# Optimization experiments

Hardware: AMD Instinct MI355X
Metric: run time of the kernel (lower is better)

Reference implementation:

```python
import jax, jax.numpy as jnp
import numpy as np

B, H, W, C = 4, 64, 64, 512
LN_EPS = 1e-3  # keras LayerNormalization default epsilon


def setup_inputs() -> dict:
    key = jax.random.key(0)
    ks = jax.random.split(key, 10)
    s = 1.0 / np.sqrt(C)
    return {
        "x": jax.random.normal(ks[0], (B, H, W, C), dtype=jnp.float32),
        "ln_g": jnp.ones((C,), jnp.float32),
        "ln_b": jnp.zeros((C,), jnp.float32),
        "Wq": jax.random.normal(ks[1], (C, C), jnp.float32) * s,
        "bq": jnp.zeros((C,), jnp.float32),
        "Wk": jax.random.normal(ks[2], (C, C), jnp.float32) * s,
        "bk": jnp.zeros((C,), jnp.float32),
        "Wv": jax.random.normal(ks[3], (C, C), jnp.float32) * s,
        "bv": jnp.zeros((C,), jnp.float32),
        "Wp": jax.random.normal(ks[4], (C, C), jnp.float32) * s,
        "bp": jnp.zeros((C,), jnp.float32),
    }


def reference(x, ln_g, ln_b, Wq, bq, Wk, bk, Wv, bv, Wp, bp):
    b, h_, w_, c = x.shape
    n = h_ * w_
    # LayerNorm over channel axis (keras default axis=-1, eps=1e-3)
    mu = jnp.mean(x, axis=-1, keepdims=True)
    var = jnp.var(x, axis=-1, keepdims=True)
    hn = (x - mu) * jax.lax.rsqrt(var + LN_EPS) * ln_g + ln_b
    hf = hn.reshape(b, n, c)
    q = hf @ Wq + bq  # [b, n, c]
    k = hf @ Wk + bk
    v = hf @ Wv + bv
    scale = 1.0 / jnp.sqrt(jnp.asarray(c, x.dtype))
    scores = jnp.einsum("bqc,bkc->bqk", q, k) * scale  # [b, n, n]
    attn = jax.nn.softmax(scores, axis=-1)
    o = jnp.einsum("bqk,bkc->bqc", attn, v)  # [b, n, c]
    o = o @ Wp + bp
    return x + o.reshape(b, h_, w_, c)
```

## Files before the change

### kernel.cpp

```cpp
#include <hip/hip_runtime.h>
#include <cstdint>
#include <cmath>

typedef unsigned short u16;
typedef __attribute__((ext_vector_type(8))) short short8;
typedef __attribute__((ext_vector_type(4))) float f32x4;

#define BB 4
#define NTOK 4096
#define CDIM 512
#define NROWS (BB * NTOK)
#define QSCALE 0.0441941738241592f

__device__ __forceinline__ u16 f2bf(float f) {
  union { float f; uint32_t u; } v; v.f = f;
  return (u16)((v.u + 0x7fffu + ((v.u >> 16) & 1u)) >> 16);
}

__device__ __forceinline__ float bf2f(u16 u) {
  union { uint32_t u; float f; } v; v.u = (uint32_t)u << 16;
  return v.f;
}

__device__ __forceinline__ f32x4 mfma16(short8 a, short8 b, f32x4 c) {
  return __builtin_amdgcn_mfma_f32_16x16x32_bf16(a, b, c, 0, 0, 0);
}

__device__ __forceinline__ void gload16(const u16* g, u16* l) {
  __builtin_amdgcn_global_load_lds(
      (const __attribute__((address_space(1))) void*)g,
      (__attribute__((address_space(3))) void*)l, 16, 0, 0);
}

__global__ __launch_bounds__(256) void ln_kernel(const float* __restrict__ x,
                                                 const float* __restrict__ gam,
                                                 const float* __restrict__ bet,
                                                 u16* __restrict__ hn) {
  int row = blockIdx.x * 4 + (threadIdx.x >> 6);
  int lane = threadIdx.x & 63;
  const float4* xr = (const float4*)(x + (size_t)row * CDIM);
  float4 a0 = xr[lane];
  float4 a1 = xr[lane + 64];
  float s = a0.x + a0.y + a0.z + a0.w + a1.x + a1.y + a1.z + a1.w;
  float ss = a0.x * a0.x + a0.y * a0.y + a0.z * a0.z + a0.w * a0.w +
             a1.x * a1.x + a1.y * a1.y + a1.z * a1.z + a1.w * a1.w;
#pragma unroll
  for (int j = 0; j < 6; ++j) {
    s += __shfl_xor(s, 1 << j);
    ss += __shfl_xor(ss, 1 << j);
  }
  float mu = s * (1.0f / CDIM);
  float var = ss * (1.0f / CDIM) - mu * mu;
  float rs = rsqrtf(var + 1e-3f);
  const float4* g4 = (const float4*)gam;
  const float4* b4 = (const float4*)bet;
  float4 g0 = g4[lane], g1 = g4[lane + 64];
  float4 c0 = b4[lane], c1 = b4[lane + 64];
  u16* out = hn + (size_t)row * CDIM;
  ushort4 o0, o1;
  o0.x = f2bf((a0.x - mu) * rs * g0.x + c0.x);
  o0.y = f2bf((a0.y - mu) * rs * g0.y + c0.y);
  o0.z = f2bf((a0.z - mu) * rs * g0.z + c0.z);
  o0.w = f2bf((a0.w - mu) * rs * g0.w + c0.w);
  o1.x = f2bf((a1.x - mu) * rs * g1.x + c1.x);
  o1.y = f2bf((a1.y - mu) * rs * g1.y + c1.y);
  o1.z = f2bf((a1.z - mu) * rs * g1.z + c1.z);
  o1.w = f2bf((a1.w - mu) * rs * g1.w + c1.w);
  *(ushort4*)(out + lane * 4) = o0;
  *(ushort4*)(out + 256 + lane * 4) = o1;
}

__global__ __launch_bounds__(256) void wconv_kernel(
    const float* __restrict__ w0, const float* __restrict__ w1,
    const float* __restrict__ w2, const float* __restrict__ w3,
    const float* __restrict__ bq, const float* __restrict__ bk,
    const float* __restrict__ bv,
    u16* __restrict__ wt, float* __restrict__ bqkv) {
  __shared__ __align__(16) u16 tile[64][65];
  int which = blockIdx.z;
  const float* W = (which == 0) ? w0 : (which == 1) ? w1 : (which == 2) ? w2 : w3;
  float wscale = (which == 0) ? QSCALE : 1.0f;
  u16* WT = wt + (size_t)which * CDIM * CDIM;
  int kb = blockIdx.x * 64, nb = blockIdx.y * 64;
  int t = threadIdx.x;
  if (kb == 0 && which < 3 && t < 64) {
    const float* bs = (which == 0) ? bq : (which == 1) ? bk : bv;
    bqkv[which * CDIM + nb + t] = bs[nb + t] * wscale;
  }
#pragma unroll
  for (int i = 0; i < 16; ++i) {
    int idx = t + i * 256;
    int r = idx >> 6, c = idx & 63;
    tile[r][c] = f2bf(W[(size_t)(kb + r) * CDIM + nb + c] * wscale);
  }
  __syncthreads();
#pragma unroll
  for (int i = 0; i < 16; ++i) {
    int idx = t + i * 256;
    int r = idx >> 6, c = idx & 63;
    WT[(size_t)(nb + r) * CDIM + kb + c] = tile[c][r];
  }
}

__global__ __launch_bounds__(256) void vtrans_kernel(const u16* __restrict__ v,
                                                     int ld,
                                                     u16* __restrict__ vt) {
  __shared__ __align__(16) u16 tile[64][65];
  int nb = blockIdx.x * 64;
  int cb = blockIdx.y * 64;
  int b = blockIdx.z;
  int t = threadIdx.x;
  const u16* src = v + ((size_t)b * NTOK + nb) * ld + cb;
#pragma unroll
  for (int i = 0; i < 16; ++i) {
    int idx = t + i * 256;
    int r = idx >> 6, c = idx & 63;
    tile[r][c] = src[(size_t)r * ld + c];
  }
  __syncthreads();
  u16* dst = vt + ((size_t)b * CDIM + cb) * NTOK + nb;
#pragma unroll
  for (int i = 0; i < 16; ++i) {
    int idx = t + i * 256;
    int r = idx >> 6, c = idx & 63;
    dst[(size_t)r * NTOK + c] = tile[c][r];
  }
}

template <int MODE, int LOGSPLIT>
__global__ __launch_bounds__(512) void gemm256_kernel(
    const u16* __restrict__ A, int lda, size_t az,
    const u16* __restrict__ Bt, int ldb, size_t bz,
    const float* __restrict__ bias,
    const float* __restrict__ lsum, int lz,
    u16* __restrict__ outp, int ldo, size_t oz, size_t koz,
    int K) {
  __shared__ __align__(16) u16 lds[8][8192];
  int t = threadIdx.x;
  int w = t >> 6, lane = t & 63;
  int lr = lane & 15, lg = lane >> 4;
  int wr = w >> 2, wc = w & 3;
  int gx = gridDim.x, gy = gridDim.y;
  int nwg = gx * gy * (int)gridDim.z;
  int nlin = blockIdx.x + gx * (blockIdx.y + gy * blockIdx.z);
  int cpx = nwg >> 3;
  int swz = (nlin & 7) * cpx + (nlin >> 3);
  int bx = swz % gx;
  int rem = swz / gx;
  int by = rem % gy;
  int bz2 = rem / gy;
  int batch = bz2 >> LOGSPLIT;
  int kq = bz2 & ((1 << LOGSPLIT) - 1);
  size_t aoff = az * (size_t)batch + (size_t)kq * K;
  size_t boff = bz * (size_t)batch + (size_t)kq * K;
  size_t ooff = oz * (size_t)batch + koz * (size_t)kq;
  int lsrow0 = lz * batch;
  int mbase = by * 256, nbase = bx * 256;
  const f32x4 fz = {0.f, 0.f, 0.f, 0.f};
  f32x4 acc[8][4];
#pragma unroll
  for (int m = 0; m < 8; ++m)
#pragma unroll
    for (int n2 = 0; n2 < 4; ++n2) acc[m][n2] = fz;

  int srow = t >> 3;
  int scol = ((t & 7) ^ (srow & 7)) * 8;
  const u16* ga = A + aoff + (size_t)(mbase + srow) * lda + scol;
  const u16* gb = Bt + boff + (size_t)(nbase + srow) * ldb + scol;
  int pse0 = (lg ^ (lr & 7)) * 8;
  int pse1 = pse0 ^ 32;

#define STG_A(h, tile, d)                                              \
  {                                                                    \
    const u16* s_ = ga + (size_t)((h)*128) * lda + (tile)*64;          \
    u16* d_ = &lds[(d)*4 + (h)][0] + w * 512;                          \
    gload16(s_, d_);                                                   \
    gload16(s_ + (size_t)64 * lda, d_ + 4096);                        \
  }
#define STG_B(h, tile, d)                                              \
  {                                                                    \
    const u16* s_ = gb + (size_t)((h)*128) * ldb + (tile)*64;          \
    u16* d_ = &lds[(d)*4 + 2 + (h)][0] + w * 512;                      \
    gload16(s_, d_);                                                   \
    gload16(s_ + (size_t)64 * ldb, d_ + 4096);                        \
  }

#define RD_A(dst, d, mh)                                               \
  {                                                                    \
    const u16* p_ = &lds[(d)*4 + wr][0] + (((mh)*64 + lr) << 6);       \
    _Pragma("unroll") for (int m = 0; m < 4; ++m) {                    \
      dst[m * 2 + 0] = *(const short8*)(p_ + (m << 10) + pse0);        \
      dst[m * 2 + 1] = *(const short8*)(p_ + (m << 10) + pse1);        \
    }                                                                  \
  }
#define RD_B(dst, d, nh)                                               \
  {                                                                    \
    const u16* p_ = &lds[(d)*4 + 2 + (wc >> 1)][0] +                   \
                    (((wc & 1) * 64 + (nh)*32 + lr) << 6);             \
    _Pragma("unroll") for (int n2 = 0; n2 < 2; ++n2) {                 \
      dst[n2 * 2 + 0] = *(const short8*)(p_ + (n2 << 10) + pse0);      \
      dst[n2 * 2 + 1] = *(const short8*)(p_ + (n2 << 10) + pse1);      \
    }                                                                  \
  }

#define PHEND                                                          \
  asm volatile("" ::: "memory");                                       \
  __builtin_amdgcn_sched_barrier(0);                                   \
  __builtin_amdgcn_s_barrier();                                        \
  asm volatile("s_waitcnt lgkmcnt(0)" ::: "memory");                   \
  __builtin_amdgcn_sched_barrier(0);

#define VM2 asm volatile("s_waitcnt vmcnt(2)" ::: "memory");
#define VM0 asm volatile("s_waitcnt vmcnt(0)" ::: "memory");

#define MM(X, Y, mq, nq)                                               \
  __builtin_amdgcn_s_setprio(1);                                       \
  _Pragma("unroll") for (int m = 0; m < 4; ++m)                        \
      _Pragma("unroll") for (int n2 = 0; n2 < 2; ++n2)                 \
          _Pragma("unroll") for (int ks = 0; ks < 2; ++ks)             \
              acc[(mq)*4 + m][(nq)*2 + n2] =                           \
                  mfma16(X[m * 2 + ks], Y[n2 * 2 + ks],                \
                         acc[(mq)*4 + m][(nq)*2 + n2]);                \
  __builtin_amdgcn_s_setprio(0);

  short8 Af[8], Ag[8], Bf[4], Bg[4];
  int niter = K >> 7;

  STG_A(0, 0, 0); STG_A(1, 0, 0); STG_B(0, 0, 0); STG_B(1, 0, 0);
  STG_B(0, 1, 1);
  VM2;
  __builtin_amdgcn_s_barrier();
  asm volatile("" ::: "memory");
  __builtin_amdgcn_sched_barrier(0);

  for (int j = 0; j < niter; ++j) {
    int T1i = 2 * j + 1, T2i = 2 * j + 2, T3i = 2 * j + 3;
    bool more = (j + 1 < niter);
    RD_A(Af, 0, 0); RD_B(Bf, 0, 0);
    STG_B(1, T1i, 1);
    PHEND; MM(Af, Bf, 0, 0);
    RD_B(Bg, 0, 1);
    STG_A(0, T1i, 1);
    PHEND; MM(Af, Bg, 0, 1);
    RD_A(Ag, 0, 1);
    STG_A(1, T1i, 1);
    PHEND; MM(Ag, Bg, 1, 1);
    if (more) { STG_B(0, T2i, 0); VM2; } else { VM0; }
    PHEND; MM(Ag, Bf, 1, 0);
    RD_A(Af, 1, 0); RD_B(Bf, 1, 0);
    if (more) STG_B(1, T2i, 0);
    PHEND; MM(Af, Bf, 0, 0);
    RD_B(Bg, 1, 1);
    if (more) STG_A(0, T2i, 0);
    PHEND; MM(Af, Bg, 0, 1);
    RD_A(Ag, 1, 1);
    if (more) STG_A(1, T2i, 0);
    PHEND; MM(Ag, Bg, 1, 1);
    if (more) { STG_B(0, T3i, 1); VM2; } else { VM0; }
    PHEND; MM(Ag, Bf, 1, 0);
  }
#undef MM
#undef VM2
#undef VM0
#undef PHEND
#undef RD_A
#undef RD_B
#undef STG_A
#undef STG_B

  u16* op = outp + ooff;
#pragma unroll
  for (int m = 0; m < 8; ++m) {
    int grow = mbase + wr * 128 + m * 16 + lg * 4;
    float rl[4];
    if (MODE == 3) {
#pragma unroll
      for (int r = 0; r < 4; ++r)
        rl[r] = 1.0f / lsum[lsrow0 + grow + r];
    }
#pragma unroll
    for (int n2 = 0; n2 < 4; ++n2) {
      int gcol = nbase + wc * 64 + n2 * 16 + lr;
      float bnc = (MODE == 0) ? bias[gcol] : 0.f;
#pragma unroll
      for (int r = 0; r < 4; ++r) {
        size_t idx = (size_t)(grow + r) * ldo + gcol;
        float val = acc[m][n2][r];
        if (MODE == 0) {
          op[idx] = f2bf(val + bnc);
        } else if (MODE == 2) {
          op[idx] = f2bf(val);
        } else {
          op[idx] = f2bf(val * rl[r]);
        }
      }
    }
  }
}

__global__ __launch_bounds__(256) void gemm_fin_kernel(
    const u16* __restrict__ A, int lda,
    const u16* __restrict__ Bt, int ldb,
    const float* __restrict__ bias, const float* __restrict__ res,
    float* __restrict__ outp, int ldo, int K) {
  __shared__ __align__(16) u16 Als[2][128 * 32];
  __shared__ __align__(16) u16 Bls[2][128 * 32];
  int t = threadIdx.x;
  int w = t >> 6, lane = t & 63;
  int lr = lane & 15, lg = lane >> 4;
  int wr = w >> 1, wc = w & 1;
  int mbase = blockIdx.y * 128, nbase = blockIdx.x * 128;
  const f32x4 fz = {0.f, 0.f, 0.f, 0.f};
  f32x4 acc[4][4];
#pragma unroll
  for (int m = 0; m < 4; ++m)
#pragma unroll
    for (int n = 0; n < 4; ++n) acc[m][n] = fz;

  int scol = (((t & 3) ^ ((t >> 2) & 3) ^ ((t >> 4) & 1)) * 8);
  const u16* ga0 = A + (size_t)(mbase + (t >> 2)) * lda + scol;
  const u16* gb0 = Bt + (size_t)(nbase + (t >> 2)) * ldb + scol;
  int rsA = (lg ^ (lr & 3) ^ ((lr >> 2) & 1)) * 8;

#define STAGE(buf, ko)                                                 \
  {                                                                    \
    gload16(ga0 + (ko), &Als[buf][w * 512]);                           \
    gload16(ga0 + (size_t)64 * lda + (ko), &Als[buf][w * 512 + 2048]); \
    gload16(gb0 + (ko), &Bls[buf][w * 512]);                           \
    gload16(gb0 + (size_t)64 * ldb + (ko), &Bls[buf][w * 512 + 2048]); \
  }

  int nk = K >> 5;
  STAGE(0, 0);
  STAGE(1, 32);
  int cur = 0;
  for (int kt = 0; kt < nk; ++kt) {
    if (kt + 1 < nk) {
      asm volatile("s_waitcnt vmcnt(4)" ::: "memory");
    } else {
      asm volatile("s_waitcnt vmcnt(0)" ::: "memory");
    }
    __builtin_amdgcn_s_barrier();
    asm volatile("" ::: "memory");
    __builtin_amdgcn_sched_barrier(0);
    short8 af[4], bfr[4];
#pragma unroll
    for (int m = 0; m < 4; ++m)
      af[m] = *(const short8*)(&Als[cur][(wr * 64 + m * 16 + lr) * 32 + rsA]);
#pragma unroll
    for (int n = 0; n < 4; ++n)
      bfr[n] = *(const short8*)(&Bls[cur][(wc * 64 + n * 16 + lr) * 32 + rsA]);
#pragma unroll
    for (int m = 0; m < 4; ++m)
#pragma unroll
      for (int n = 0; n < 4; ++n)
        acc[m][n] = mfma16(af[m], bfr[n], acc[m][n]);
    asm volatile("s_waitcnt lgkmcnt(0)" ::: "memory");
    __builtin_amdgcn_s_barrier();
    asm volatile("" ::: "memory");
    if (kt + 2 < nk) STAGE(cur, (kt + 2) * 32);
    cur ^= 1;
  }
#undef STAGE

#pragma unroll
  for (int m = 0; m < 4; ++m) {
    int grow = mbase + wr * 64 + m * 16 + lg * 4;
#pragma unroll
    for (int n = 0; n < 4; ++n) {
      int gcol = nbase + wc * 64 + n * 16 + lr;
      float bnc = bias[gcol];
#pragma unroll
      for (int r = 0; r < 4; ++r) {
        size_t idx = (size_t)(grow + r) * ldo + gcol;
        outp[idx] = acc[m][n][r] + bnc + res[idx];
      }
    }
  }
}

__global__ __launch_bounds__(256) void softmax_kernel(u16* __restrict__ S,
                                                      float* __restrict__ lsum) {
  int row = blockIdx.x * 4 + (threadIdx.x >> 6);
  int lane = threadIdx.x & 63;
  u16* Sr = S + (size_t)row * NTOK;
  short8 d[8];
#pragma unroll
  for (int i = 0; i < 8; ++i)
    d[i] = *(const short8*)(Sr + i * 512 + lane * 8);
  float mx = -1e30f;
#pragma unroll
  for (int i = 0; i < 8; ++i)
#pragma unroll
    for (int j = 0; j < 8; ++j) mx = fmaxf(mx, bf2f((u16)d[i][j]));
#pragma unroll
  for (int j = 0; j < 6; ++j) mx = fmaxf(mx, __shfl_xor(mx, 1 << j));
  float sum = 0.f;
#pragma unroll
  for (int i = 0; i < 8; ++i) {
    short8 o;
#pragma unroll
    for (int j = 0; j < 8; ++j) {
      float p = __expf(bf2f((u16)d[i][j]) - mx);
      sum += p;
      o[j] = (short)f2bf(p);
    }
    *(short8*)(Sr + i * 512 + lane * 8) = o;
  }
#pragma unroll
  for (int j = 0; j < 6; ++j) sum += __shfl_xor(sum, 1 << j);
  if (lane == 0) lsum[row] = sum;
}

__global__ __launch_bounds__(256) void addp2_kernel(const u16* __restrict__ p,
                                                    size_t ss,
                                                    u16* __restrict__ ob) {
  size_t i = ((size_t)blockIdx.x * 256 + threadIdx.x) * 8;
  short8 a0 = *(const short8*)(p + i);
  short8 a1 = *(const short8*)(p + ss + i);
  short8 o;
#pragma unroll
  for (int j = 0; j < 8; ++j)
    o[j] = (short)f2bf(bf2f((u16)a0[j]) + bf2f((u16)a1[j]));
  *(short8*)(ob + i) = o;
}

extern "C" void kernel_launch(void* const* d_in, const int* in_sizes, int n_in,
                              void* d_out, int out_size, void* d_ws, size_t ws_size,
                              hipStream_t stream) {
  (void)in_sizes; (void)n_in; (void)out_size;
  const float* x    = (const float*)d_in[0];
  const float* ln_g = (const float*)d_in[1];
  const float* ln_b = (const float*)d_in[2];
  const float* Wq   = (const float*)d_in[3];
  const float* bq   = (const float*)d_in[4];
  const float* Wk   = (const float*)d_in[5];
  const float* bk   = (const float*)d_in[6];
  const float* Wv   = (const float*)d_in[7];
  const float* bv   = (const float*)d_in[8];
  const float* Wp   = (const float*)d_in[9];
  const float* bp   = (const float*)d_in[10];

  const size_t MB = 1024ull * 1024ull;
  const size_t KB = 1024ull;
  char* ws = (char*)d_ws;
  u16* wt     = (u16*)(ws);
  float* bqkv = (float*)(ws + 2 * MB);
  float* ls   = (float*)(ws + 2 * MB + 64 * KB);
  u16* hn     = (u16*)(ws + 4 * MB);
  u16* qkv    = (u16*)(ws + 20 * MB);
  u16* vt     = (u16*)(ws + 68 * MB);
  bool full = ws_size >= 212 * MB;
  u16* S    = (u16*)(ws + 84 * MB);
  u16* part = (u16*)(ws + 4 * MB);
  u16* ob   = full ? vt : (u16*)(ws + 116 * MB);

  const float* nullf = nullptr;

  hipLaunchKernelGGL(wconv_kernel, dim3(8, 8, 4), dim3(256), 0, stream,
                     Wq, Wk, Wv, Wp, bq, bk, bv, wt, bqkv);
  hipLaunchKernelGGL(ln_kernel, dim3(NROWS / 4), dim3(256), 0, stream,
                     x, ln_g, ln_b, hn);
  hipLaunchKernelGGL((gemm256_kernel<0, 0>), dim3(6, 64, 1), dim3(512), 0,
                     stream, hn, CDIM, (size_t)0, wt, CDIM, (size_t)0,
                     bqkv, nullf, 0, qkv, 3 * CDIM, (size_t)0, (size_t)0, CDIM);
  hipLaunchKernelGGL(vtrans_kernel, dim3(64, 8, 4), dim3(256), 0, stream,
                     qkv + 2 * CDIM, 3 * CDIM, vt);

  if (full) {
    hipLaunchKernelGGL((gemm256_kernel<2, 0>), dim3(16, 16, 4), dim3(512), 0,
                       stream, qkv, 3 * CDIM, (size_t)NTOK * 3 * CDIM,
                       qkv + CDIM, 3 * CDIM, (size_t)NTOK * 3 * CDIM,
                       nullf, nullf, 0,
                       S, NTOK, (size_t)NTOK * NTOK, (size_t)0, CDIM);
    hipLaunchKernelGGL(softmax_kernel, dim3(4 * NTOK / 4), dim3(256), 0, stream,
                       S, ls);
    hipLaunchKernelGGL((gemm256_kernel<3, 1>), dim3(2, 16, 8), dim3(512), 0,
                       stream, S, NTOK, (size_t)NTOK * NTOK,
                       vt, NTOK, (size_t)CDIM * NTOK,
                       nullf, ls, NTOK,
                       part, CDIM, (size_t)NTOK * CDIM,
                       (size_t)NROWS * CDIM, NTOK / 2);
    hipLaunchKernelGGL(addp2_kernel, dim3(NROWS * CDIM / 2048), dim3(256), 0,
                       stream, part, (size_t)NROWS * CDIM, ob);
  } else {
    for (int p = 0; p < 4; ++p) {
      const u16* qp  = qkv + (size_t)p * NTOK * 3 * CDIM;
      const u16* kp  = qp + CDIM;
      const u16* vtp = vt + (size_t)p * CDIM * NTOK;
      u16* obp = ob + (size_t)p * NTOK * CDIM;
      float* lp = ls + (size_t)p * NTOK;
      hipLaunchKernelGGL((gemm256_kernel<2, 0>), dim3(16, 16, 1), dim3(512), 0,
                         stream, qp, 3 * CDIM, (size_t)0, kp, 3 * CDIM,
                         (size_t)0, nullf, nullf, 0,
                         S, NTOK, (size_t)0, (size_t)0, CDIM);
      hipLaunchKernelGGL(softmax_kernel, dim3(NTOK / 4), dim3(256), 0, stream,
                         S, lp);
      hipLaunchKernelGGL((gemm256_kernel<3, 0>), dim3(2, 16, 1), dim3(512), 0,
                         stream, S, NTOK, (size_t)0, vtp, NTOK, (size_t)0,
                         nullf, lp, 0,
                         obp, CDIM, (size_t)0, (size_t)0, NTOK);
    }
  }
  hipLaunchKernelGGL(gemm_fin_kernel, dim3(4, 128), dim3(256), 0, stream,
                     ob, CDIM, wt + 3 * CDIM * CDIM, CDIM,
                     bp, x, (float*)d_out, CDIM, CDIM);
}
```

Before: 278.9 us.

## Fold output projection into V weights and fuse softmax exp into QK GEMM epilogue

Precomputes Wv·Wp in a small GEMM so the V projection produces already-projected values. This removes the final output-projection GEMM, and the split-K reduction kernel now also adds the bias and residual. The QK^T GEMM epilogue applies exp directly, with no max subtraction, and writes per-tile partial row sums. A small reduction kernel then combines those sums, which removes the separate softmax pass over the full score matrix. Skipping the max subtraction risks overflow when scores are large, and folding the weights changes the rounding order.

```diff
diff --git a/kernel.cpp b/kernel.cpp
--- a/kernel.cpp
+++ b/kernel.cpp
@@ -10,6 +10,7 @@
 #define NTOK 4096
 #define CDIM 512
 #define NROWS (BB * NTOK)
+#define SLOT ((size_t)CDIM * CDIM)
 #define QSCALE 0.0441941738241592f
 
 __device__ __forceinline__ u16 f2bf(float f) {
@@ -74,18 +75,28 @@
     const float* __restrict__ w0, const float* __restrict__ w1,
     const float* __restrict__ w2, const float* __restrict__ w3,
     const float* __restrict__ bq, const float* __restrict__ bk,
-    const float* __restrict__ bv,
     u16* __restrict__ wt, float* __restrict__ bqkv) {
   __shared__ __align__(16) u16 tile[64][65];
   int which = blockIdx.z;
   const float* W = (which == 0) ? w0 : (which == 1) ? w1 : (which == 2) ? w2 : w3;
   float wscale = (which == 0) ? QSCALE : 1.0f;
-  u16* WT = wt + (size_t)which * CDIM * CDIM;
+  const int slotmap[4] = {2, 3, 0, 1};
+  u16* WT = wt + (size_t)slotmap[which] * SLOT;
   int kb = blockIdx.x * 64, nb = blockIdx.y * 64;
   int t = threadIdx.x;
-  if (kb == 0 && which < 3 && t < 64) {
-    const float* bs = (which == 0) ? bq : (which == 1) ? bk : bv;
+  if (kb == 0 && which < 2 && t < 64) {
+    const float* bs = (which == 0) ? bq : bk;
     bqkv[which * CDIM + nb + t] = bs[nb + t] * wscale;
+  }
+  if (which == 2) {
+#pragma unroll
+    for (int i = 0; i < 16; ++i) {
+      int idx = t + i * 256;
+      int r = idx >> 6, c = idx & 63;
+      WT[(size_t)(kb + r) * CDIM + nb + c] =
+          f2bf(W[(size_t)(kb + r) * CDIM + nb + c]);
+    }
+    return;
   }
 #pragma unroll
   for (int i = 0; i < 16; ++i) {
@@ -100,6 +111,15 @@
     int r = idx >> 6, c = idx & 63;
     WT[(size_t)(nb + r) * CDIM + kb + c] = tile[c][r];
   }
+}
+
+__global__ __launch_bounds__(256) void bvp_kernel(const float* __restrict__ bv,
+                                                  const float* __restrict__ Wp,
+                                                  float* __restrict__ bqkv) {
+  int m = blockIdx.x * 256 + threadIdx.x;
+  float s = 0.f;
+  for (int k = 0; k < CDIM; ++k) s += bv[k] * Wp[(size_t)k * CDIM + m];
+  bqkv[2 * CDIM + m] = s;
 }
 
 __global__ __launch_bounds__(256) void vtrans_kernel(const u16* __restrict__ v,
@@ -132,7 +152,7 @@
     const u16* __restrict__ A, int lda, size_t az,
     const u16* __restrict__ Bt, int ldb, size_t bz,
     const float* __restrict__ bias,
-    const float* __restrict__ lsum, int lz,
+    float* __restrict__ lsum, int lz,
     u16* __restrict__ outp, int ldo, size_t oz, size_t koz,
     int K) {
   __shared__ __align__(16) u16 lds[8][8192];
@@ -269,6 +289,35 @@
 #undef STG_B
 
   u16* op = outp + ooff;
+  if (MODE == 2) {
+    __syncthreads();
+    float* redf = (float*)&lds[0][0];
+#pragma unroll
+    for (int m = 0; m < 8; ++m) {
+#pragma unroll
+      for (int r = 0; r < 4; ++r) {
+        int rowl = wr * 128 + m * 16 + lg * 4 + r;
+        float part = 0.f;
+#pragma unroll
+        for (int n2 = 0; n2 < 4; ++n2) {
+          int gcol = nbase + wc * 64 + n2 * 16 + lr;
+          float p = __expf(acc[m][n2][r]);
+          u16 pb = f2bf(p);
+          op[(size_t)(mbase + rowl) * ldo + gcol] = pb;
+          part += bf2f(pb);
+        }
+        redf[rowl * 65 + wc * 16 + lr] = part;
+      }
+    }
+    __syncthreads();
+    if (t < 256) {
+      float s = 0.f;
+#pragma unroll 8
+      for (int j2 = 0; j2 < 64; ++j2) s += redf[t * 65 + j2];
+      lsum[((size_t)bx * gridDim.z + batch) * (size_t)lz + mbase + t] = s;
+    }
+    return;
+  }
 #pragma unroll
   for (int m = 0; m < 8; ++m) {
     int grow = mbase + wr * 128 + m * 16 + lg * 4;
@@ -288,8 +337,6 @@
         float val = acc[m][n2][r];
         if (MODE == 0) {
           op[idx] = f2bf(val + bnc);
-        } else if (MODE == 2) {
-          op[idx] = f2bf(val);
         } else {
           op[idx] = f2bf(val * rl[r]);
         }
@@ -298,11 +345,9 @@
   }
 }
 
-__global__ __launch_bounds__(256) void gemm_fin_kernel(
-    const u16* __restrict__ A, int lda,
-    const u16* __restrict__ Bt, int ldb,
-    const float* __restrict__ bias, const float* __restrict__ res,
-    float* __restrict__ outp, int ldo, int K) {
+__global__ __launch_bounds__(256) void gemm_w_kernel(
+    const u16* __restrict__ A, const u16* __restrict__ Bt,
+    u16* __restrict__ outp) {
   __shared__ __align__(16) u16 Als[2][128 * 32];
   __shared__ __align__(16) u16 Bls[2][128 * 32];
   int t = threadIdx.x;
@@ -318,19 +363,19 @@
     for (int n = 0; n < 4; ++n) acc[m][n] = fz;
 
   int scol = (((t & 3) ^ ((t >> 2) & 3) ^ ((t >> 4) & 1)) * 8);
-  const u16* ga0 = A + (size_t)(mbase + (t >> 2)) * lda + scol;
-  const u16* gb0 = Bt + (size_t)(nbase + (t >> 2)) * ldb + scol;
+  const u16* ga0 = A + (size_t)(mbase + (t >> 2)) * CDIM + scol;
+  const u16* gb0 = Bt + (size_t)(nbase + (t >> 2)) * CDIM + scol;
   int rsA = (lg ^ (lr & 3) ^ ((lr >> 2) & 1)) * 8;
 
-#define STAGE(buf, ko)                                                 \
-  {                                                                    \
-    gload16(ga0 + (ko), &Als[buf][w * 512]);                           \
-    gload16(ga0 + (size_t)64 * lda + (ko), &Als[buf][w * 512 + 2048]); \
-    gload16(gb0 + (ko), &Bls[buf][w * 512]);                           \
-    gload16(gb0 + (size_t)64 * ldb + (ko), &Bls[buf][w * 512 + 2048]); \
-  }
-
-  int nk = K >> 5;
+#define STAGE(buf, ko)                                                  \
+  {                                                                     \
+    gload16(ga0 + (ko), &Als[buf][w * 512]);                            \
+    gload16(ga0 + (size_t)64 * CDIM + (ko), &Als[buf][w * 512 + 2048]); \
+    gload16(gb0 + (ko), &Bls[buf][w * 512]);                            \
+    gload16(gb0 + (size_t)64 * CDIM + (ko), &Bls[buf][w * 512 + 2048]); \
+  }
+
+  int nk = CDIM >> 5;
   STAGE(0, 0);
   STAGE(1, 32);
   int cur = 0;
@@ -369,60 +414,35 @@
 #pragma unroll
     for (int n = 0; n < 4; ++n) {
       int gcol = nbase + wc * 64 + n * 16 + lr;
-      float bnc = bias[gcol];
-#pragma unroll
-      for (int r = 0; r < 4; ++r) {
-        size_t idx = (size_t)(grow + r) * ldo + gcol;
-        outp[idx] = acc[m][n][r] + bnc + res[idx];
-      }
-    }
-  }
-}
-
-__global__ __launch_bounds__(256) void softmax_kernel(u16* __restrict__ S,
-                                                      float* __restrict__ lsum) {
-  int row = blockIdx.x * 4 + (threadIdx.x >> 6);
-  int lane = threadIdx.x & 63;
-  u16* Sr = S + (size_t)row * NTOK;
-  short8 d[8];
-#pragma unroll
-  for (int i = 0; i < 8; ++i)
-    d[i] = *(const short8*)(Sr + i * 512 + lane * 8);
-  float mx = -1e30f;
-#pragma unroll
-  for (int i = 0; i < 8; ++i)
-#pragma unroll
-    for (int j = 0; j < 8; ++j) mx = fmaxf(mx, bf2f((u16)d[i][j]));
-#pragma unroll
-  for (int j = 0; j < 6; ++j) mx = fmaxf(mx, __shfl_xor(mx, 1 << j));
-  float sum = 0.f;
-#pragma unroll
-  for (int i = 0; i < 8; ++i) {
-    short8 o;
-#pragma unroll
-    for (int j = 0; j < 8; ++j) {
-      float p = __expf(bf2f((u16)d[i][j]) - mx);
-      sum += p;
-      o[j] = (short)f2bf(p);
-    }
-    *(short8*)(Sr + i * 512 + lane * 8) = o;
-  }
-#pragma unroll
-  for (int j = 0; j < 6; ++j) sum += __shfl_xor(sum, 1 << j);
-  if (lane == 0) lsum[row] = sum;
-}
-
-__global__ __launch_bounds__(256) void addp2_kernel(const u16* __restrict__ p,
-                                                    size_t ss,
-                                                    u16* __restrict__ ob) {
+#pragma unroll
+      for (int r = 0; r < 4; ++r)
+        outp[(size_t)(grow + r) * CDIM + gcol] = f2bf(acc[m][n][r]);
+    }
+  }
+}
+
+__global__ __launch_bounds__(256) void lred_kernel(const float* __restrict__ lsp,
+                                                   float* __restrict__ ls,
+                                                   size_t stride) {
+  size_t r = (size_t)blockIdx.x * 256 + threadIdx.x;
+  float s = 0.f;
+#pragma unroll
+  for (int b = 0; b < 16; ++b) s += lsp[b * stride + r];
+  ls[r] = s;
+}
+
+__global__ __launch_bounds__(256) void addfin_kernel(const u16* __restrict__ p,
+                                                     size_t ss,
+                                                     const float* __restrict__ bp,
+                                                     const float* __restrict__ x,
+                                                     float* __restrict__ out) {
   size_t i = ((size_t)blockIdx.x * 256 + threadIdx.x) * 8;
   short8 a0 = *(const short8*)(p + i);
   short8 a1 = *(const short8*)(p + ss + i);
-  short8 o;
+  int col = (int)(i & (CDIM - 1));
 #pragma unroll
   for (int j = 0; j < 8; ++j)
-    o[j] = (short)f2bf(bf2f((u16)a0[j]) + bf2f((u16)a1[j]));
-  *(short8*)(ob + i) = o;
+    out[i + j] = bf2f((u16)a0[j]) + bf2f((u16)a1[j]) + bp[col + j] + x[i + j];
 }
 
 extern "C" void kernel_launch(void* const* d_in, const int* in_sizes, int n_in,
@@ -445,25 +465,30 @@
   const size_t KB = 1024ull;
   char* ws = (char*)d_ws;
   u16* wt     = (u16*)(ws);
-  float* bqkv = (float*)(ws + 2 * MB);
-  float* ls   = (float*)(ws + 2 * MB + 64 * KB);
+  float* bqkv = (float*)(ws + 2 * MB + 512 * KB);
+  float* ls   = (float*)(ws + 2 * MB + 768 * KB);
+  float* lsp  = (float*)(ws + 3 * MB);
   u16* hn     = (u16*)(ws + 4 * MB);
   u16* qkv    = (u16*)(ws + 20 * MB);
   u16* vt     = (u16*)(ws + 68 * MB);
   bool full = ws_size >= 212 * MB;
   u16* S    = (u16*)(ws + 84 * MB);
   u16* part = (u16*)(ws + 4 * MB);
-  u16* ob   = full ? vt : (u16*)(ws + 116 * MB);
+  u16* pnf  = (u16*)(ws + 116 * MB);
 
   const float* nullf = nullptr;
+  float* nullm = nullptr;
 
   hipLaunchKernelGGL(wconv_kernel, dim3(8, 8, 4), dim3(256), 0, stream,
-                     Wq, Wk, Wv, Wp, bq, bk, bv, wt, bqkv);
+                     Wq, Wk, Wv, Wp, bq, bk, wt, bqkv);
+  hipLaunchKernelGGL(gemm_w_kernel, dim3(4, 4), dim3(256), 0, stream,
+                     wt + 1 * SLOT, wt + 0 * SLOT, wt + 4 * SLOT);
+  hipLaunchKernelGGL(bvp_kernel, dim3(2), dim3(256), 0, stream, bv, Wp, bqkv);
   hipLaunchKernelGGL(ln_kernel, dim3(NROWS / 4), dim3(256), 0, stream,
                      x, ln_g, ln_b, hn);
   hipLaunchKernelGGL((gemm256_kernel<0, 0>), dim3(6, 64, 1), dim3(512), 0,
-                     stream, hn, CDIM, (size_t)0, wt, CDIM, (size_t)0,
-                     bqkv, nullf, 0, qkv, 3 * CDIM, (size_t)0, (size_t)0, CDIM);
+                     stream, hn, CDIM, (size_t)0, wt + 2 * SLOT, CDIM, (size_t)0,
+                     bqkv, nullm, 0, qkv, 3 * CDIM, (size_t)0, (size_t)0, CDIM);
   hipLaunchKernelGGL(vtrans_kernel, dim3(64, 8, 4), dim3(256), 0, stream,
                      qkv + 2 * CDIM, 3 * CDIM, vt);
 
@@ -471,38 +496,38 @@
     hipLaunchKernelGGL((gemm256_kernel<2, 0>), dim3(16, 16, 4), dim3(512), 0,
                        stream, qkv, 3 * CDIM, (size_t)NTOK * 3 * CDIM,
                        qkv + CDIM, 3 * CDIM, (size_t)NTOK * 3 * CDIM,
-                       nullf, nullf, 0,
+                       nullf, lsp, NTOK,
                        S, NTOK, (size_t)NTOK * NTOK, (size_t)0, CDIM);
-    hipLaunchKernelGGL(softmax_kernel, dim3(4 * NTOK / 4), dim3(256), 0, stream,
-                       S, ls);
+    hipLaunchKernelGGL(lred_kernel, dim3(NROWS / 256), dim3(256), 0, stream,
+                       lsp, ls, (size_t)NROWS);
     hipLaunchKernelGGL((gemm256_kernel<3, 1>), dim3(2, 16, 8), dim3(512), 0,
                        stream, S, NTOK, (size_t)NTOK * NTOK,
                        vt, NTOK, (size_t)CDIM * NTOK,
                        nullf, ls, NTOK,
                        part, CDIM, (size_t)NTOK * CDIM,
                        (size_t)NROWS * CDIM, NTOK / 2);
-    hipLaunchKernelGGL(addp2_kernel, dim3(NROWS * CDIM / 2048), dim3(256), 0,
-                       stream, part, (size_t)NROWS * CDIM, ob);
+    hipLaunchKernelGGL(addfin_kernel, dim3(NROWS * CDIM / 2048), dim3(256), 0,
+                       stream, part, (size_t)NROWS * CDIM, bp, x,
+                       (float*)d_out);
   } else {
     for (int p = 0; p < 4; ++p) {
       const u16* qp  = qkv + (size_t)p * NTOK * 3 * CDIM;
       const u16* kp  = qp + CDIM;
       const u16* vtp = vt + (size_t)p * CDIM * NTOK;
-      u16* obp = ob + (size_t)p * NTOK * CDIM;
-      float* lp = ls + (size_t)p * NTOK;
       hipLaunchKernelGGL((gemm256_kernel<2, 0>), dim3(16, 16, 1), dim3(512), 0,
                          stream, qp, 3 * CDIM, (size_t)0, kp, 3 * CDIM,
-                         (size_t)0, nullf, nullf, 0,
+                         (size_t)0, nullf, lsp, NTOK,
                          S, NTOK, (size_t)0, (size_t)0, CDIM);
-      hipLaunchKernelGGL(softmax_kernel, dim3(NTOK / 4), dim3(256), 0, stream,
-                         S, lp);
-      hipLaunchKernelGGL((gemm256_kernel<3, 0>), dim3(2, 16, 1), dim3(512), 0,
+      hipLaunchKernelGGL(lred_kernel, dim3(NTOK / 256), dim3(256), 0, stream,
+                         lsp, ls, (size_t)NTOK);
+      hipLaunchKernelGGL((gemm256_kernel<3, 1>), dim3(2, 16, 2), dim3(512), 0,
                          stream, S, NTOK, (size_t)0, vtp, NTOK, (size_t)0,
-                         nullf, lp, 0,
-                         obp, CDIM, (size_t)0, (size_t)0, NTOK);
-    }
-  }
-  hipLaunchKernelGGL(gemm_fin_kernel, dim3(4, 128), dim3(256), 0, stream,
-                     ob, CDIM, wt + 3 * CDIM * CDIM, CDIM,
-                     bp, x, (float*)d_out, CDIM, CDIM);
-}
+                         nullf, ls, 0,
+                         pnf, CDIM, (size_t)0, (size_t)NTOK * CDIM, NTOK / 2);
+      hipLaunchKernelGGL(addfin_kernel, dim3(NTOK * CDIM / 2048), dim3(256), 0,
+                         stream, pnf, (size_t)NTOK * CDIM, bp,
+                         x + (size_t)p * NTOK * CDIM,
+                         (float*)d_out + (size_t)p * NTOK * CDIM);
+    }
+  }
+}
```

New measurement: 258.0 us. 7.5% less time.
